# Optimization experiments

Hardware: AMD Instinct MI355X
Metric: run time of the kernel (lower is better)

Reference implementation:

```python
import jax, jax.numpy as jnp
import numpy as np

KH, KW = 3, 3  # kernel_size


def _median_patches(x):
    """tf.image.extract_patches(SAME, stride 1) + top_k median over k*k*C values.
    Returns [B, H, W, 1] with the (D//2+1)-th largest value per window (D = KH*KW*C),
    exactly matching tf.nn.top_k(..., k=D//2+1).values[..., -1]."""
    B, H, W, C = x.shape
    ph, pw = KH - 1, KW - 1  # SAME padding, stride 1
    xp = jnp.pad(x, ((0, 0), (ph // 2, ph - ph // 2), (pw // 2, pw - pw // 2), (0, 0)))
    # [B, H, W, KH*KW, C] via shifted slices (zero-padded borders, like TF SAME)
    patches = jnp.stack(
        [xp[:, i:i + H, j:j + W, :] for i in range(KH) for j in range(KW)], axis=3
    )
    D = KH * KW * C
    patches = patches.reshape(B, H, W, D)
    # k-th largest with k = D//2 + 1  ->  ascending-sorted index D - (D//2 + 1)
    med_idx = D - (D // 2) - 1
    med = jnp.sort(patches, axis=-1)[..., med_idx]
    return med[..., None]


def setup_inputs() -> dict:
    key = jax.random.key(0)
    kx, kw = jax.random.split(key)
    x = jax.random.normal(kx, (32, 224, 224, 3), dtype=jnp.float32)
    W = jax.random.normal(kw, (KH, KW, 1, 64), dtype=jnp.float32) * 0.1  # HWIO, in_ch=1
    return {"x": x, "W": W}


def reference(x, W):
    med = _median_patches(x)                              # [B, H, W, 1]
    med = med - jnp.mean(med, axis=(0, 1, 2), keepdims=True)  # global mean-center
    out = jax.lax.conv_general_dilated(
        med, W, window_strides=(1, 1), padding="SAME",
        dimension_numbers=("NHWC", "HWIO", "NHWC"),
    )                                                      # [B, H, W, num_filters]
    return out
```

## Files before the change

kernel.cpp:

```cpp
#include <hip/hip_runtime.h>

#define BB 32
#define HH 224
#define WW 224
#define CC 3
#define FF 64
#define NPIX (BB * HH * WW)

#define PH 226
#define PW 228
#define PB (PH * PW)
#define NPAD (BB * PB)

typedef float f32x4 __attribute__((ext_vector_type(4)));
typedef float f32x4u __attribute__((ext_vector_type(4), aligned(4)));

#define CEX(A,B) { const float _lo = fminf(A,B); B = fmaxf(A,B); A = _lo; }

__global__ __launch_bounds__(128) void median_pad_kernel(const float* __restrict__ x,
                                                         float* __restrict__ cmed,
                                                         float* __restrict__ partial) {
    const int bid = blockIdx.x;
    const int b  = bid / 56;
    const int hg = bid % 56;
    const int lr = threadIdx.x >> 5;
    const int s  = threadIdx.x & 31;
    const int w0 = s * 7;
    const int h  = hg * 4 + lr;

    __shared__ float xs[6][680];
    {
        const int h0 = hg * 4 - 1;
        for (int t = threadIdx.x; t < 1008; t += 128) {
            const int rr = t / 168, i = t % 168;
            const int hin = h0 + rr;
            f32x4 v = {0.f, 0.f, 0.f, 0.f};
            if (hin >= 0 && hin < HH) {
                v = *(const f32x4*)(x + (((long long)b * HH + hin) * WW) * CC + i * 4);
            }
            *(f32x4*)&xs[rr][4 + i * 4] = v;
        }
        if (threadIdx.x < 48) {
            const int rr = threadIdx.x >> 3, k = threadIdx.x & 7;
            xs[rr][(k < 4) ? k : (672 + k)] = 0.f;
        }
    }
    __syncthreads();

    float col[9][9];

#define COLSTEP(CS) { \
    const int cb = 4 + (w0 - 1 + (CS)) * 3; \
    float a0 = xs[lr][cb+0],   a1 = xs[lr][cb+1],   a2 = xs[lr][cb+2]; \
    float b0 = xs[lr+1][cb+0], b1 = xs[lr+1][cb+1], b2 = xs[lr+1][cb+2]; \
    float c0 = xs[lr+2][cb+0], c1 = xs[lr+2][cb+1], c2 = xs[lr+2][cb+2]; \
    CEX(a0,a1); CEX(a1,a2); CEX(a0,a1); \
    CEX(b0,b1); CEX(b1,b2); CEX(b0,b1); \
    CEX(c0,c1); CEX(c1,c2); CEX(c0,c1); \
    float s0 = a0, L = b0; CEX(s0, L); \
    float s5 = b2, Hh = a2; CEX(Hh, s5); \
    float q0 = L, q1 = a1, q2 = b1, q3 = Hh; \
    CEX(q0,q1); CEX(q2,q3); CEX(q0,q2); CEX(q1,q3); CEX(q1,q2); \
    float z0 = s0, p = c0; CEX(z0, p); \
    float z8 = c2, qq = s5; CEX(qq, z8); \
    float t0 = p, t1 = c1, t2 = qq; CEX(t0,t1); CEX(t1,t2); CEX(t0,t1); \
    float m1 = q0, u = t0; CEX(m1, u); \
    float m7 = t2, vvv = q3; CEX(vvv, m7); \
    float e0 = u, e1 = q1, e2 = q2; CEX(e0,e1); CEX(e1,e2); \
    float f0 = t1, f1 = e0, f2 = e1, f3 = e2; CEX(f0,f1); CEX(f1,f2); CEX(f2,f3); \
    float g0 = vvv, g1 = f0, g2 = f1, g3 = f2, g4 = f3; \
    CEX(g0,g1); CEX(g1,g2); CEX(g2,g3); CEX(g3,g4); \
    col[CS][0]=z0; col[CS][1]=m1; col[CS][2]=g0; col[CS][3]=g1; col[CS][4]=g2; \
    col[CS][5]=g3; col[CS][6]=g4; col[CS][7]=m7; col[CS][8]=z8; }

    COLSTEP(0) COLSTEP(1) COLSTEP(2) COLSTEP(3) COLSTEP(4)
    COLSTEP(5) COLSTEP(6) COLSTEP(7) COLSTEP(8)

    float med[7];
    float lsum = 0.f;

#define MEDSTEP(O) { \
    float x0 = col[O][0], y0 = col[O+2][0]; CEX(x0, y0); \
    float x8 = col[O][8], y8 = col[O+2][8]; CEX(x8, y8); \
    float g0 = y0, g1 = col[O][1], g2 = col[O][2], g3 = col[O][3], \
          g4 = col[O][4], g5 = col[O][5], g6 = col[O][6], g7 = col[O][7]; \
    CEX(g0,g1); CEX(g1,g2); CEX(g2,g3); CEX(g3,g4); CEX(g4,g5); CEX(g5,g6); CEX(g6,g7); \
    float h0 = col[O+2][1], h1 = col[O+2][2], h2 = col[O+2][3], h3 = col[O+2][4], \
          h4 = col[O+2][5], h5 = col[O+2][6], h6 = col[O+2][7], h7 = x8; \
    CEX(h6,h7); CEX(h5,h6); CEX(h4,h5); CEX(h3,h4); CEX(h2,h3); CEX(h1,h2); CEX(h0,h1); \
    float Ea = g0, Eb = g4, Ec = h0, Ed = h4; \
    float Ea2 = g2, Eb2 = g6, Ec2 = h2, Ed2 = h6; \
    CEX(Ea,Ec); CEX(Eb,Ed); CEX(Eb,Ec); \
    CEX(Ea2,Ec2); CEX(Eb2,Ed2); CEX(Eb2,Ec2); \
    CEX(Ea2,Eb); CEX(Eb2,Ec); CEX(Ec2,Ed); \
    float Fa = g1, Fb = g5, Fc = h1, Fd = h5; \
    float Fa2 = g3, Fb2 = g7, Fc2 = h3, Fd2 = h7; \
    CEX(Fa,Fc); CEX(Fb,Fd); CEX(Fb,Fc); \
    CEX(Fa2,Fc2); CEX(Fb2,Fd2); CEX(Fb2,Fc2); \
    CEX(Fa2,Fb); CEX(Fb2,Fc); CEX(Fc2,Fd); \
    float M3 = Fa2, M4 = Eb;  CEX(M3, M4); \
    float M5 = Fb,  M6 = Eb2; CEX(M5, M6); \
    float M7 = Fb2, M8 = Ec;  CEX(M7, M8); \
    float M9 = Fc,  M10 = Ec2; CEX(M9, M10); \
    float M11 = Fc2, M12 = Ed; CEX(M11, M12); \
    float r = fminf(fmaxf(M3, col[O+1][8]), fmaxf(M4, col[O+1][7])); \
    r = fminf(r, fmaxf(M5, col[O+1][6])); \
    r = fminf(r, fmaxf(M6, col[O+1][5])); \
    r = fminf(r, fmaxf(M7, col[O+1][4])); \
    r = fminf(r, fmaxf(M8, col[O+1][3])); \
    r = fminf(r, fmaxf(M9, col[O+1][2])); \
    r = fminf(r, fmaxf(M10, col[O+1][1])); \
    r = fminf(r, fmaxf(M11, col[O+1][0])); \
    r = fminf(r, M12); \
    med[O] = r; lsum += r; }

    MEDSTEP(0) MEDSTEP(1) MEDSTEP(2) MEDSTEP(3) MEDSTEP(4) MEDSTEP(5) MEDSTEP(6)

    float* crow = cmed + ((long long)b * PH + (h + 1)) * PW + (w0 + 1);
    crow[0] = med[0]; crow[1] = med[1]; crow[2] = med[2]; crow[3] = med[3];
    crow[4] = med[4]; crow[5] = med[5]; crow[6] = med[6];

    __shared__ float sdata[128];
    sdata[threadIdx.x] = lsum;
    __syncthreads();
    #pragma unroll
    for (int st = 64; st > 0; st >>= 1) {
        if (threadIdx.x < st) sdata[threadIdx.x] += sdata[threadIdx.x + st];
        __syncthreads();
    }
    if (threadIdx.x == 0) partial[blockIdx.x] = sdata[0];
}

__global__ __launch_bounds__(256) void mean_wsum_border_kernel(const float* __restrict__ partial,
                                                               const float* __restrict__ Wt,
                                                               float* __restrict__ mean_out,
                                                               float* __restrict__ Asum,
                                                               float* __restrict__ cmed) {
    if (blockIdx.x == 0) {
        if (threadIdx.x < FF) {
            float s = 0.0f;
            #pragma unroll
            for (int t = 0; t < 9; ++t) s += Wt[t * FF + threadIdx.x];
            Asum[threadIdx.x] = s;
        }
        float s = 0.0f;
        for (int i = threadIdx.x; i < 1792; i += 256) s += partial[i];
        __shared__ float sdata[256];
        sdata[threadIdx.x] = s;
        __syncthreads();
        #pragma unroll
        for (int st = 128; st > 0; st >>= 1) {
            if (threadIdx.x < st) sdata[threadIdx.x] += sdata[threadIdx.x + st];
            __syncthreads();
        }
        if (threadIdx.x == 0) mean_out[0] = sdata[0] / (float)NPIX;
    } else {
        const int u = (blockIdx.x - 1) * 256 + threadIdx.x;
        int b, hp, wp;
        if (u < 14592) {
            b = u / 456;
            const int v = u % 456;
            hp = (v < 228) ? 0 : (PH - 1);
            wp = (v < 228) ? v : (v - 228);
        } else {
            const int u2 = u - 14592;
            b = u2 / 896;
            const int v2 = u2 % 896;
            hp = 1 + (v2 % 224);
            const int j = v2 / 224;
            wp = (j == 0) ? 0 : (224 + j);
        }
        cmed[((long long)b * PH + hp) * PW + wp] = 0.0f;
    }
}

__global__ __launch_bounds__(256) void conv_kernel(const float* __restrict__ cmed,
                                                   const float* __restrict__ Wt,
                                                   const float* __restrict__ Asum,
                                                   const float* __restrict__ mean_p,
                                                   float* __restrict__ out) {
    const int bid = blockIdx.x;
    const int h  = bid % HH;
    const int b  = bid / HH;

    const int fg = threadIdx.x & 15;
    const int pg = threadIdx.x >> 4;
    const int f4 = fg * 4;

    float w[9][4];
    #pragma unroll
    for (int t = 0; t < 9; ++t) {
        const f32x4u wv = *(const f32x4u*)(Wt + t * FF + f4);
        w[t][0] = wv.x; w[t][1] = wv.y; w[t][2] = wv.z; w[t][3] = wv.w;
    }
    const f32x4u Av = *(const f32x4u*)(Asum + f4);
    const float mean = mean_p[0];

    const float* base = cmed + ((long long)b * PH + h) * PW;
    f32x4u cv[7][3];
    #pragma unroll
    for (int it = 0; it < 7; ++it) {
        #pragma unroll
        for (int r = 0; r < 3; ++r) {
            cv[it][r] = *(const f32x4u*)(base + r * PW + it * 32 + pg * 2);
        }
    }

    float Sb[4] = {Av.x, Av.y, Av.z, Av.w};
    if (h == 0) {
        #pragma unroll
        for (int k = 0; k < 4; ++k) Sb[k] -= (w[0][k] + w[1][k] + w[2][k]);
    }
    if (h == HH - 1) {
        #pragma unroll
        for (int k = 0; k < 4; ++k) Sb[k] -= (w[6][k] + w[7][k] + w[8][k]);
    }

    float* orow = out + (((long long)b * HH + h) * WW) * FF + f4;

    #pragma unroll
    for (int it = 0; it < 7; ++it) {
        const int p = it * 32 + pg * 2;

        float acc0[4] = {0.f, 0.f, 0.f, 0.f};
        float acc1[4] = {0.f, 0.f, 0.f, 0.f};
        #pragma unroll
        for (int r = 0; r < 3; ++r) {
            const f32x4u cvv = cv[it][r];
            #pragma unroll
            for (int k = 0; k < 4; ++k) {
                acc0[k] = fmaf(cvv.x, w[r * 3 + 0][k], acc0[k]);
                acc0[k] = fmaf(cvv.y, w[r * 3 + 1][k], acc0[k]);
                acc0[k] = fmaf(cvv.z, w[r * 3 + 2][k], acc0[k]);
                acc1[k] = fmaf(cvv.y, w[r * 3 + 0][k], acc1[k]);
                acc1[k] = fmaf(cvv.z, w[r * 3 + 1][k], acc1[k]);
                acc1[k] = fmaf(cvv.w, w[r * 3 + 2][k], acc1[k]);
            }
        }

        float S0[4], S1[4];
        #pragma unroll
        for (int k = 0; k < 4; ++k) { S0[k] = Sb[k]; S1[k] = Sb[k]; }
        if (it == 0 && pg == 0) {
            #pragma unroll
            for (int k = 0; k < 4; ++k) {
                S0[k] -= (w[0][k] + w[3][k] + w[6][k]);
                if (h == 0)      S0[k] += w[0][k];
                if (h == HH - 1) S0[k] += w[6][k];
            }
        }
        if (it == 6 && pg == 15) {
            #pragma unroll
            for (int k = 0; k < 4; ++k) {
                S1[k] -= (w[2][k] + w[5][k] + w[8][k]);
                if (h == 0)      S1[k] += w[2][k];
                if (h == HH - 1) S1[k] += w[8][k];
            }
        }

        f32x4 o0, o1;
        o0.x = fmaf(-mean, S0[0], acc0[0]); o0.y = fmaf(-mean, S0[1], acc0[1]);
        o0.z = fmaf(-mean, S0[2], acc0[2]); o0.w = fmaf(-mean, S0[3], acc0[3]);
        o1.x = fmaf(-mean, S1[0], acc1[0]); o1.y = fmaf(-mean, S1[1], acc1[1]);
        o1.z = fmaf(-mean, S1[2], acc1[2]); o1.w = fmaf(-mean, S1[3], acc1[3]);

        float* op = orow + (long long)p * FF;
        *(f32x4*)op = o0;
        *(f32x4*)(op + FF) = o1;
    }
}

extern "C" void kernel_launch(void* const* d_in, const int* in_sizes, int n_in,
                              void* d_out, int out_size, void* d_ws, size_t ws_size,
                              hipStream_t stream) {
    const float* x  = (const float*)d_in[0];
    const float* Wt = (const float*)d_in[1];
    float* out = (float*)d_out;

    float* cmed    = (float*)d_ws;
    float* Asum    = cmed + NPAD;
    float* partial = Asum + FF;
    float* mean_p  = partial + 1792;

    median_pad_kernel<<<1792, 128, 0, stream>>>(x, cmed, partial);
    mean_wsum_border_kernel<<<170, 256, 0, stream>>>(partial, Wt, mean_p, Asum, cmed);
    conv_kernel<<<BB * HH, 256, 0, stream>>>(cmed, Wt, Asum, mean_p, out);
}
```

Measured before the change: 105.6 us.

## Fold border zeroing into median kernel and process four rows per conv block

Moves zeroing of the padded cmed border from the mean/wsum kernel into the median kernel, so the reduction kernel runs as a single block. The conv kernel now handles four output rows per block (1792 blocks instead of 7168), so the weights and Asum are loaded once per four rows. This reduces per-block setup overhead, but each block has more serial work and fewer blocks are available to spread across the GPU.

```diff
diff --git a/kernel.cpp b/kernel.cpp
--- a/kernel.cpp
+++ b/kernel.cpp
@@ -27,6 +27,21 @@
     const int s  = threadIdx.x & 31;
     const int w0 = s * 7;
     const int h  = hg * 4 + lr;
+
+    if (threadIdx.x < 16) {
+        const int rr = threadIdx.x >> 2;
+        const int cc = threadIdx.x & 3;
+        const int wp = (cc == 0) ? 0 : (224 + cc);
+        cmed[((long long)b * PH + (hg * 4 + rr + 1)) * PW + wp] = 0.0f;
+    }
+    if (hg == 0) {
+        for (int t = threadIdx.x; t < PW; t += 128)
+            cmed[((long long)b * PH) * PW + t] = 0.0f;
+    }
+    if (hg == 55) {
+        for (int t = threadIdx.x; t < PW; t += 128)
+            cmed[((long long)b * PH + (PH - 1)) * PW + t] = 0.0f;
+    }
 
     __shared__ float xs[6][680];
     {
@@ -131,47 +146,27 @@
     if (threadIdx.x == 0) partial[blockIdx.x] = sdata[0];
 }
 
-__global__ __launch_bounds__(256) void mean_wsum_border_kernel(const float* __restrict__ partial,
-                                                               const float* __restrict__ Wt,
-                                                               float* __restrict__ mean_out,
-                                                               float* __restrict__ Asum,
-                                                               float* __restrict__ cmed) {
-    if (blockIdx.x == 0) {
-        if (threadIdx.x < FF) {
-            float s = 0.0f;
-            #pragma unroll
-            for (int t = 0; t < 9; ++t) s += Wt[t * FF + threadIdx.x];
-            Asum[threadIdx.x] = s;
-        }
+__global__ __launch_bounds__(256) void mean_wsum_kernel(const float* __restrict__ partial,
+                                                        const float* __restrict__ Wt,
+                                                        float* __restrict__ mean_out,
+                                                        float* __restrict__ Asum) {
+    if (threadIdx.x < FF) {
         float s = 0.0f;
-        for (int i = threadIdx.x; i < 1792; i += 256) s += partial[i];
-        __shared__ float sdata[256];
-        sdata[threadIdx.x] = s;
+        #pragma unroll
+        for (int t = 0; t < 9; ++t) s += Wt[t * FF + threadIdx.x];
+        Asum[threadIdx.x] = s;
+    }
+    float s = 0.0f;
+    for (int i = threadIdx.x; i < 1792; i += 256) s += partial[i];
+    __shared__ float sdata[256];
+    sdata[threadIdx.x] = s;
+    __syncthreads();
+    #pragma unroll
+    for (int st = 128; st > 0; st >>= 1) {
+        if (threadIdx.x < st) sdata[threadIdx.x] += sdata[threadIdx.x + st];
         __syncthreads();
-        #pragma unroll
-        for (int st = 128; st > 0; st >>= 1) {
-            if (threadIdx.x < st) sdata[threadIdx.x] += sdata[threadIdx.x + st];
-            __syncthreads();
-        }
-        if (threadIdx.x == 0) mean_out[0] = sdata[0] / (float)NPIX;
-    } else {
-        const int u = (blockIdx.x - 1) * 256 + threadIdx.x;
-        int b, hp, wp;
-        if (u < 14592) {
-            b = u / 456;
-            const int v = u % 456;
-            hp = (v < 228) ? 0 : (PH - 1);
-            wp = (v < 228) ? v : (v - 228);
-        } else {
-            const int u2 = u - 14592;
-            b = u2 / 896;
-            const int v2 = u2 % 896;
-            hp = 1 + (v2 % 224);
-            const int j = v2 / 224;
-            wp = (j == 0) ? 0 : (224 + j);
-        }
-        cmed[((long long)b * PH + hp) * PW + wp] = 0.0f;
-    }
+    }
+    if (threadIdx.x == 0) mean_out[0] = sdata[0] / (float)NPIX;
 }
 
 __global__ __launch_bounds__(256) void conv_kernel(const float* __restrict__ cmed,
@@ -180,8 +175,8 @@
                                                    const float* __restrict__ mean_p,
                                                    float* __restrict__ out) {
     const int bid = blockIdx.x;
-    const int h  = bid % HH;
-    const int b  = bid / HH;
+    const int b  = bid / 56;
+    const int h0 = (bid % 56) * 4;
 
     const int fg = threadIdx.x & 15;
     const int pg = threadIdx.x >> 4;
@@ -196,77 +191,82 @@
     const f32x4u Av = *(const f32x4u*)(Asum + f4);
     const float mean = mean_p[0];
 
-    const float* base = cmed + ((long long)b * PH + h) * PW;
-    f32x4u cv[7][3];
-    #pragma unroll
-    for (int it = 0; it < 7; ++it) {
+    #pragma unroll
+    for (int rr = 0; rr < 4; ++rr) {
+        const int h = h0 + rr;
+
+        const float* base = cmed + ((long long)b * PH + h) * PW;
+        f32x4u cv[7][3];
         #pragma unroll
-        for (int r = 0; r < 3; ++r) {
-            cv[it][r] = *(const f32x4u*)(base + r * PW + it * 32 + pg * 2);
-        }
-    }
-
-    float Sb[4] = {Av.x, Av.y, Av.z, Av.w};
-    if (h == 0) {
+        for (int it = 0; it < 7; ++it) {
+            #pragma unroll
+            for (int r = 0; r < 3; ++r) {
+                cv[it][r] = *(const f32x4u*)(base + r * PW + it * 32 + pg * 2);
+            }
+        }
+
+        float Sb[4] = {Av.x, Av.y, Av.z, Av.w};
+        if (h == 0) {
+            #pragma unroll
+            for (int k = 0; k < 4; ++k) Sb[k] -= (w[0][k] + w[1][k] + w[2][k]);
+        }
+        if (h == HH - 1) {
+            #pragma unroll
+            for (int k = 0; k < 4; ++k) Sb[k] -= (w[6][k] + w[7][k] + w[8][k]);
+        }
+
+        float* orow = out + (((long long)b * HH + h) * WW) * FF + f4;
+
         #pragma unroll
-        for (int k = 0; k < 4; ++k) Sb[k] -= (w[0][k] + w[1][k] + w[2][k]);
-    }
-    if (h == HH - 1) {
-        #pragma unroll
-        for (int k = 0; k < 4; ++k) Sb[k] -= (w[6][k] + w[7][k] + w[8][k]);
-    }
-
-    float* orow = out + (((long long)b * HH + h) * WW) * FF + f4;
-
-    #pragma unroll
-    for (int it = 0; it < 7; ++it) {
-        const int p = it * 32 + pg * 2;
-
-        float acc0[4] = {0.f, 0.f, 0.f, 0.f};
-        float acc1[4] = {0.f, 0.f, 0.f, 0.f};
-        #pragma unroll
-        for (int r = 0; r < 3; ++r) {
-            const f32x4u cvv = cv[it][r];
-            #pragma unroll
-            for (int k = 0; k < 4; ++k) {
-                acc0[k] = fmaf(cvv.x, w[r * 3 + 0][k], acc0[k]);
-                acc0[k] = fmaf(cvv.y, w[r * 3 + 1][k], acc0[k]);
-                acc0[k] = fmaf(cvv.z, w[r * 3 + 2][k], acc0[k]);
-                acc1[k] = fmaf(cvv.y, w[r * 3 + 0][k], acc1[k]);
-                acc1[k] = fmaf(cvv.z, w[r * 3 + 1][k], acc1[k]);
-                acc1[k] = fmaf(cvv.w, w[r * 3 + 2][k], acc1[k]);
-            }
-        }
-
-        float S0[4], S1[4];
-        #pragma unroll
-        for (int k = 0; k < 4; ++k) { S0[k] = Sb[k]; S1[k] = Sb[k]; }
-        if (it == 0 && pg == 0) {
-            #pragma unroll
-            for (int k = 0; k < 4; ++k) {
-                S0[k] -= (w[0][k] + w[3][k] + w[6][k]);
-                if (h == 0)      S0[k] += w[0][k];
-                if (h == HH - 1) S0[k] += w[6][k];
-            }
-        }
-        if (it == 6 && pg == 15) {
-            #pragma unroll
-            for (int k = 0; k < 4; ++k) {
-                S1[k] -= (w[2][k] + w[5][k] + w[8][k]);
-                if (h == 0)      S1[k] += w[2][k];
-                if (h == HH - 1) S1[k] += w[8][k];
-            }
-        }
-
-        f32x4 o0, o1;
-        o0.x = fmaf(-mean, S0[0], acc0[0]); o0.y = fmaf(-mean, S0[1], acc0[1]);
-        o0.z = fmaf(-mean, S0[2], acc0[2]); o0.w = fmaf(-mean, S0[3], acc0[3]);
-        o1.x = fmaf(-mean, S1[0], acc1[0]); o1.y = fmaf(-mean, S1[1], acc1[1]);
-        o1.z = fmaf(-mean, S1[2], acc1[2]); o1.w = fmaf(-mean, S1[3], acc1[3]);
-
-        float* op = orow + (long long)p * FF;
-        *(f32x4*)op = o0;
-        *(f32x4*)(op + FF) = o1;
+        for (int it = 0; it < 7; ++it) {
+            const int p = it * 32 + pg * 2;
+
+            float acc0[4] = {0.f, 0.f, 0.f, 0.f};
+            float acc1[4] = {0.f, 0.f, 0.f, 0.f};
+            #pragma unroll
+            for (int r = 0; r < 3; ++r) {
+                const f32x4u cvv = cv[it][r];
+                #pragma unroll
+                for (int k = 0; k < 4; ++k) {
+                    acc0[k] = fmaf(cvv.x, w[r * 3 + 0][k], acc0[k]);
+                    acc0[k] = fmaf(cvv.y, w[r * 3 + 1][k], acc0[k]);
+                    acc0[k] = fmaf(cvv.z, w[r * 3 + 2][k], acc0[k]);
+                    acc1[k] = fmaf(cvv.y, w[r * 3 + 0][k], acc1[k]);
+                    acc1[k] = fmaf(cvv.z, w[r * 3 + 1][k], acc1[k]);
+                    acc1[k] = fmaf(cvv.w, w[r * 3 + 2][k], acc1[k]);
+                }
+            }
+
+            float S0[4], S1[4];
+            #pragma unroll
+            for (int k = 0; k < 4; ++k) { S0[k] = Sb[k]; S1[k] = Sb[k]; }
+            if (it == 0 && pg == 0) {
+                #pragma unroll
+                for (int k = 0; k < 4; ++k) {
+                    S0[k] -= (w[0][k] + w[3][k] + w[6][k]);
+                    if (h == 0)      S0[k] += w[0][k];
+                    if (h == HH - 1) S0[k] += w[6][k];
+                }
+            }
+            if (it == 6 && pg == 15) {
+                #pragma unroll
+                for (int k = 0; k < 4; ++k) {
+                    S1[k] -= (w[2][k] + w[5][k] + w[8][k]);
+                    if (h == 0)      S1[k] += w[2][k];
+                    if (h == HH - 1) S1[k] += w[8][k];
+                }
+            }
+
+            f32x4 o0, o1;
+            o0.x = fmaf(-mean, S0[0], acc0[0]); o0.y = fmaf(-mean, S0[1], acc0[1]);
+            o0.z = fmaf(-mean, S0[2], acc0[2]); o0.w = fmaf(-mean, S0[3], acc0[3]);
+            o1.x = fmaf(-mean, S1[0], acc1[0]); o1.y = fmaf(-mean, S1[1], acc1[1]);
+            o1.z = fmaf(-mean, S1[2], acc1[2]); o1.w = fmaf(-mean, S1[3], acc1[3]);
+
+            float* op = orow + (long long)p * FF;
+            *(f32x4*)op = o0;
+            *(f32x4*)(op + FF) = o1;
+        }
     }
 }
 
@@ -283,6 +283,6 @@
     float* mean_p  = partial + 1792;
 
     median_pad_kernel<<<1792, 128, 0, stream>>>(x, cmed, partial);
-    mean_wsum_border_kernel<<<170, 256, 0, stream>>>(partial, Wt, mean_p, Asum, cmed);
-    conv_kernel<<<BB * HH, 256, 0, stream>>>(cmed, Wt, Asum, mean_p, out);
-}
+    mean_wsum_kernel<<<1, 256, 0, stream>>>(partial, Wt, mean_p, Asum);
+    conv_kernel<<<1792, 256, 0, stream>>>(cmed, Wt, Asum, mean_p, out);
+}
```

Measured after the change: 108.4 us. 2.6% more time.
